# Kernel optimization log

Hardware: AMD Instinct MI355X
Metric: run time of the kernel (lower is better)

Reference implementation:

```python
import math
import jax, jax.numpy as jnp
import numpy as np

THETA = 2.0 ** 16
TWO_PI = 2.0 * math.pi


def _freqs(N):
    # quantize(arange(N), 2) = floor(t/2)*2 -> paired frequencies
    idx = jnp.floor(jnp.arange(N, dtype=jnp.float32) / 2.0) * 2.0
    return 1.0 / (THETA ** (idx / N)) / TWO_PI  # (N,)


def _rope(v, cos, sin):
    # rotate pairs: (-v_odd, v_even) interleaved back to original layout
    v_rot = jnp.stack((-v[..., 1::2], v[..., ::2]), axis=-1).reshape(v.shape)
    return v * cos + v_rot * sin


def setup_inputs() -> dict:
    key = jax.random.key(0)
    k1, k2 = jax.random.split(key)
    B, nh, T, N, D = 1, 4, 2048, 8192, 256
    Q = jax.random.normal(k1, (B, nh, T, N), dtype=jnp.float32) * 0.02
    V = jax.random.normal(k2, (B, 1, T, D), dtype=jnp.float32)
    return {"Q": Q, "V": V}


def reference(Q, V):
    # Q: (B, nh, T, N) sparse neuron space; V: (B, 1, T, D) embedding space; K is Q
    T, N = Q.shape[2], Q.shape[3]
    freqs = _freqs(N)
    phases = jnp.arange(T, dtype=jnp.float32)[:, None] * freqs[None, :]  # (T, N)
    ang = (phases % 1.0) * TWO_PI
    cos, sin = jnp.cos(ang), jnp.sin(ang)
    QR = _rope(Q, cos, sin)  # (B, nh, T, N)
    scores = jnp.einsum('bhtn,bhsn->bhts', QR, QR)  # (B, nh, T, T)
    causal = jnp.tril(jnp.ones((T, T), dtype=bool), k=-1)  # strictly lower
    scores = jnp.where(causal, scores, 0.0)
    # V broadcasts over heads: (B, nh, T, T) @ (B, 1, T, D) -> (B, nh, T, D)
    return jnp.matmul(scores, V)
```

## Files before the change

kernel.cpp:

```cpp
#include <hip/hip_runtime.h>

#define LDS_AS __attribute__((address_space(3)))
#define GLB_AS __attribute__((address_space(1)))

typedef __attribute__((ext_vector_type(8))) short bf16x8;
typedef __attribute__((ext_vector_type(4))) float f32x4;

static constexpr int NH = 4;
static constexpr int T  = 2048;
static constexpr int N  = 8192;
static constexpr int D  = 256;

__device__ inline unsigned short f2bf(float f) {
    unsigned int u = __float_as_uint(f);
    u += 0x7FFFu + ((u >> 16) & 1u);
    return (unsigned short)(u >> 16);
}

__device__ inline void gl2lds16(const void* g, void* l) {
    __builtin_amdgcn_global_load_lds((GLB_AS void*)g, (LDS_AS void*)l, 16, 0, 0);
}

__global__ void rope_kernel(const float* __restrict__ Q, unsigned short* __restrict__ QR) {
    int g = blockIdx.x * 256 + threadIdx.x;
    int base = g << 2;
    int n = base & (N - 1);
    int t = (base >> 13) & (T - 1);
    const float4 q = *(const float4*)(Q + (size_t)base);
    float tf = (float)t;
    const float inv2pi = 0.15915494309189535f;
    float f0 = exp2f((float)n       * (-1.0f / 512.0f)) * inv2pi;
    float f1 = exp2f((float)(n + 2) * (-1.0f / 512.0f)) * inv2pi;
    float r0 = tf * f0; r0 -= floorf(r0);
    float r1 = tf * f1; r1 -= floorf(r1);
    float s0 = __builtin_amdgcn_sinf(r0), c0 = __builtin_amdgcn_cosf(r0);
    float s1 = __builtin_amdgcn_sinf(r1), c1 = __builtin_amdgcn_cosf(r1);
    ushort4 o;
    o.x = f2bf(q.x * c0 - q.y * s0);
    o.y = f2bf(q.y * c0 + q.x * s0);
    o.z = f2bf(q.z * c1 - q.w * s1);
    o.w = f2bf(q.w * c1 + q.z * s1);
    *(ushort4*)(QR + (size_t)base) = o;
}

__global__ void vt_kernel(const float* __restrict__ V, unsigned short* __restrict__ Vt) {
    int g = blockIdx.x * 256 + threadIdx.x;
    int t = g >> 8;
    int d = g & (D - 1);
    Vt[(size_t)d * T + t] = f2bf(V[g]);
}

__global__ __launch_bounds__(256) void gemm1_kernel(const unsigned short* __restrict__ QR,
                                                    unsigned short* __restrict__ S) {
    __shared__ __align__(16) unsigned short As[128 * 32];
    __shared__ __align__(16) unsigned short Bs[128 * 32];

    int bx = blockIdx.x;
    int h = bx / 136, pair = bx % 136;
    int bi = 0;
    while (((bi + 1) * (bi + 2)) / 2 <= pair) bi++;
    int bj = pair - (bi * (bi + 1)) / 2;

    const unsigned short* A = QR + (size_t)h * T * N + (size_t)bi * 128 * N;
    const unsigned short* B = QR + (size_t)h * T * N + (size_t)bj * 128 * N;

    int tid = threadIdx.x;
    int lane = tid & 63, wave = tid >> 6;
    int wm = wave >> 1, wn = wave & 1;
    int quad = lane >> 4, l16 = lane & 15;
    int srow = tid >> 2;
    int scol = (tid & 3) * 8;

    f32x4 acc[4][4];
    #pragma unroll
    for (int i = 0; i < 4; i++)
        #pragma unroll
        for (int j = 0; j < 4; j++)
            #pragma unroll
            for (int r = 0; r < 4; r++) acc[i][j][r] = 0.0f;

    for (int k0 = 0; k0 < N; k0 += 32) {
        __syncthreads();
        gl2lds16(A + (size_t)srow * N + k0 + scol,        &As[srow * 32 + scol]);
        gl2lds16(A + (size_t)(srow + 64) * N + k0 + scol, &As[(srow + 64) * 32 + scol]);
        gl2lds16(B + (size_t)srow * N + k0 + scol,        &Bs[srow * 32 + scol]);
        gl2lds16(B + (size_t)(srow + 64) * N + k0 + scol, &Bs[(srow + 64) * 32 + scol]);
        __syncthreads();

        bf16x8 a[4], b[4];
        #pragma unroll
        for (int i = 0; i < 4; i++) {
            int ra = wm * 64 + i * 16 + l16;
            a[i] = *(const bf16x8*)&As[ra * 32 + quad * 8];
            int rb = wn * 64 + i * 16 + l16;
            b[i] = *(const bf16x8*)&Bs[rb * 32 + quad * 8];
        }
        #pragma unroll
        for (int i = 0; i < 4; i++)
            #pragma unroll
            for (int j = 0; j < 4; j++)
                acc[i][j] = __builtin_amdgcn_mfma_f32_16x16x32_bf16(a[i], b[j], acc[i][j], 0, 0, 0);
    }

    unsigned short* Sh = S + (size_t)h * T * T;
    #pragma unroll
    for (int i = 0; i < 4; i++) {
        int t_base = bi * 128 + wm * 64 + i * 16 + quad * 4;
        #pragma unroll
        for (int j = 0; j < 4; j++) {
            int s_g = bj * 128 + wn * 64 + j * 16 + l16;
            #pragma unroll
            for (int r = 0; r < 4; r++) {
                int t_g = t_base + r;
                float v = (s_g < t_g) ? acc[i][j][r] : 0.0f;
                Sh[(size_t)t_g * T + s_g] = f2bf(v);
            }
        }
    }
}

__global__ __launch_bounds__(256) void gemm2_kernel(const unsigned short* __restrict__ S,
                                                    const unsigned short* __restrict__ Vt,
                                                    float* __restrict__ out) {
    __shared__ __align__(16) unsigned short As[128 * 32];
    __shared__ __align__(16) unsigned short Bs[128 * 32];

    int bx = blockIdx.x;
    int h = bx >> 5;
    int rem = bx & 31;
    int bi = rem >> 1;
    int dblk = rem & 1;

    const unsigned short* A = S + (size_t)h * T * T + (size_t)bi * 128 * T;
    const unsigned short* B = Vt + (size_t)dblk * 128 * T;

    int tid = threadIdx.x;
    int lane = tid & 63, wave = tid >> 6;
    int wm = wave >> 1, wn = wave & 1;
    int quad = lane >> 4, l16 = lane & 15;
    int srow = tid >> 2;
    int scol = (tid & 3) * 8;

    f32x4 acc[4][4];
    #pragma unroll
    for (int i = 0; i < 4; i++)
        #pragma unroll
        for (int j = 0; j < 4; j++)
            #pragma unroll
            for (int r = 0; r < 4; r++) acc[i][j][r] = 0.0f;

    int kend = (bi + 1) * 128;
    for (int k0 = 0; k0 < kend; k0 += 32) {
        __syncthreads();
        gl2lds16(A + (size_t)srow * T + k0 + scol,        &As[srow * 32 + scol]);
        gl2lds16(A + (size_t)(srow + 64) * T + k0 + scol, &As[(srow + 64) * 32 + scol]);
        gl2lds16(B + (size_t)srow * T + k0 + scol,        &Bs[srow * 32 + scol]);
        gl2lds16(B + (size_t)(srow + 64) * T + k0 + scol, &Bs[(srow + 64) * 32 + scol]);
        __syncthreads();

        bf16x8 a[4], b[4];
        #pragma unroll
        for (int i = 0; i < 4; i++) {
            int ra = wm * 64 + i * 16 + l16;
            a[i] = *(const bf16x8*)&As[ra * 32 + quad * 8];
            int rb = wn * 64 + i * 16 + l16;
            b[i] = *(const bf16x8*)&Bs[rb * 32 + quad * 8];
        }
        #pragma unroll
        for (int i = 0; i < 4; i++)
            #pragma unroll
            for (int j = 0; j < 4; j++)
                acc[i][j] = __builtin_amdgcn_mfma_f32_16x16x32_bf16(a[i], b[j], acc[i][j], 0, 0, 0);
    }

    float* oh = out + (size_t)h * T * D;
    #pragma unroll
    for (int i = 0; i < 4; i++) {
        int t_base = bi * 128 + wm * 64 + i * 16 + quad * 4;
        #pragma unroll
        for (int j = 0; j < 4; j++) {
            int d_g = dblk * 128 + wn * 64 + j * 16 + l16;
            #pragma unroll
            for (int r = 0; r < 4; r++) {
                int t_g = t_base + r;
                oh[(size_t)t_g * D + d_g] = acc[i][j][r];
            }
        }
    }
}

extern "C" void kernel_launch(void* const* d_in, const int* in_sizes, int n_in,
                              void* d_out, int out_size, void* d_ws, size_t ws_size,
                              hipStream_t stream) {
    const float* Q = (const float*)d_in[0];
    const float* V = (const float*)d_in[1];
    float* out = (float*)d_out;

    const size_t qr_elems = (size_t)NH * T * N;
    const size_t vt_elems = (size_t)D * T;
    const size_t s_elems  = (size_t)NH * T * T;
    const size_t needed = (qr_elems + vt_elems + s_elems) * sizeof(unsigned short);
    if (ws_size < needed) return;

    unsigned short* QR = (unsigned short*)d_ws;
    unsigned short* Vt = QR + qr_elems;
    unsigned short* S  = Vt + vt_elems;

    rope_kernel<<<(NH * T * N / 4) / 256, 256, 0, stream>>>(Q, QR);
    vt_kernel<<<(T * D) / 256, 256, 0, stream>>>(V, Vt);
    gemm1_kernel<<<NH * 136, 256, 0, stream>>>(QR, S);
    gemm2_kernel<<<NH * 32, 256, 0, stream>>>(S, Vt, out);
}
```

Baseline: 646.9 us.

## Split-K both GEMMs with atomic accumulation and tile the V transpose through LDS

gemm1 now splits the N reduction into KS chunks. Each chunk writes a separate bf16 partial score matrix, which raises the block count from 544 to 1088 on a 256-CU part. gemm2 splits each row block's causal K range into 512-wide chunks and also sums over the KS partials, accumulating into a zeroed output with float atomicAdd to give more parallelism than the original 128 blocks. The V transpose goes through a padded LDS tile so that global accesses coalesce. The cost is double the S workspace traffic, an extra memset, and atomic contention. Each partial is also rounded to bf16 separately, which changes numerics slightly.

```diff
diff --git a/kernel.cpp b/kernel.cpp
--- a/kernel.cpp
+++ b/kernel.cpp
@@ -44,25 +44,45 @@
 }
 
 __global__ void vt_kernel(const float* __restrict__ V, unsigned short* __restrict__ Vt) {
-    int g = blockIdx.x * 256 + threadIdx.x;
-    int t = g >> 8;
-    int d = g & (D - 1);
-    Vt[(size_t)d * T + t] = f2bf(V[g]);
+    __shared__ unsigned short tile[64 * 65];
+    int tb = blockIdx.x >> 2, db = blockIdx.x & 3;
+    int t0 = tb * 64, d0 = db * 64;
+    int tid = threadIdx.x;
+    #pragma unroll
+    for (int r = 0; r < 16; r++) {
+        int idx = tid + r * 256;
+        int tl = idx >> 6, dl = idx & 63;
+        tile[tl * 65 + dl] = f2bf(V[(size_t)(t0 + tl) * D + d0 + dl]);
+    }
+    __syncthreads();
+    #pragma unroll
+    for (int r = 0; r < 16; r++) {
+        int idx = tid + r * 256;
+        int dl = idx >> 6, tl = idx & 63;
+        Vt[(size_t)(d0 + dl) * T + t0 + tl] = tile[tl * 65 + dl];
+    }
 }
 
 __global__ __launch_bounds__(256) void gemm1_kernel(const unsigned short* __restrict__ QR,
-                                                    unsigned short* __restrict__ S) {
+                                                    unsigned short* __restrict__ S, int KS) {
     __shared__ __align__(16) unsigned short As[128 * 32];
     __shared__ __align__(16) unsigned short Bs[128 * 32];
 
     int bx = blockIdx.x;
-    int h = bx / 136, pair = bx % 136;
+    int per_h = 136 * KS;
+    int h = bx / per_h;
+    int rem = bx % per_h;
+    int pair = rem / KS;
+    int ks = rem % KS;
     int bi = 0;
     while (((bi + 1) * (bi + 2)) / 2 <= pair) bi++;
     int bj = pair - (bi * (bi + 1)) / 2;
 
     const unsigned short* A = QR + (size_t)h * T * N + (size_t)bi * 128 * N;
     const unsigned short* B = QR + (size_t)h * T * N + (size_t)bj * 128 * N;
+
+    int KN = N / KS;
+    int k_begin = ks * KN, k_end = k_begin + KN;
 
     int tid = threadIdx.x;
     int lane = tid & 63, wave = tid >> 6;
@@ -79,7 +99,7 @@
             #pragma unroll
             for (int r = 0; r < 4; r++) acc[i][j][r] = 0.0f;
 
-    for (int k0 = 0; k0 < N; k0 += 32) {
+    for (int k0 = k_begin; k0 < k_end; k0 += 32) {
         __syncthreads();
         gl2lds16(A + (size_t)srow * N + k0 + scol,        &As[srow * 32 + scol]);
         gl2lds16(A + (size_t)(srow + 64) * N + k0 + scol, &As[(srow + 64) * 32 + scol]);
@@ -90,10 +110,8 @@
         bf16x8 a[4], b[4];
         #pragma unroll
         for (int i = 0; i < 4; i++) {
-            int ra = wm * 64 + i * 16 + l16;
-            a[i] = *(const bf16x8*)&As[ra * 32 + quad * 8];
-            int rb = wn * 64 + i * 16 + l16;
-            b[i] = *(const bf16x8*)&Bs[rb * 32 + quad * 8];
+            a[i] = *(const bf16x8*)&As[(wm * 64 + i * 16 + l16) * 32 + quad * 8];
+            b[i] = *(const bf16x8*)&Bs[(wn * 64 + i * 16 + l16) * 32 + quad * 8];
         }
         #pragma unroll
         for (int i = 0; i < 4; i++)
@@ -102,7 +120,7 @@
                 acc[i][j] = __builtin_amdgcn_mfma_f32_16x16x32_bf16(a[i], b[j], acc[i][j], 0, 0, 0);
     }
 
-    unsigned short* Sh = S + (size_t)h * T * T;
+    unsigned short* Sh = S + (size_t)ks * NH * T * T + (size_t)h * T * T;
     #pragma unroll
     for (int i = 0; i < 4; i++) {
         int t_base = bi * 128 + wm * 64 + i * 16 + quad * 4;
@@ -121,18 +139,29 @@
 
 __global__ __launch_bounds__(256) void gemm2_kernel(const unsigned short* __restrict__ S,
                                                     const unsigned short* __restrict__ Vt,
-                                                    float* __restrict__ out) {
+                                                    float* __restrict__ out, int KS) {
     __shared__ __align__(16) unsigned short As[128 * 32];
     __shared__ __align__(16) unsigned short Bs[128 * 32];
 
     int bx = blockIdx.x;
-    int h = bx >> 5;
-    int rem = bx & 31;
-    int bi = rem >> 1;
-    int dblk = rem & 1;
-
-    const unsigned short* A = S + (size_t)h * T * T + (size_t)bi * 128 * T;
-    const unsigned short* B = Vt + (size_t)dblk * 128 * T;
+    int per_h = 2 * KS * 40;
+    int h = bx / per_h;
+    int rem = bx % per_h;
+    int dblk = rem / (KS * 40);
+    int rem2 = rem % (KS * 40);
+    int ks = rem2 / 40;
+    int tc = rem2 % 40;
+    int bi = 0, cum = 0;
+    for (; bi < 16; bi++) { int nc = (bi + 4) >> 2; if (cum + nc > tc) break; cum += nc; }
+    int c = tc - cum;
+
+    int kend = (bi + 1) * 128;
+    int cstart = c * 512;
+    int clen = min(512, kend - cstart);
+
+    const unsigned short* A = S + (size_t)ks * NH * T * T + (size_t)h * T * T
+                                + (size_t)bi * 128 * T + cstart;
+    const unsigned short* B = Vt + (size_t)dblk * 128 * T + cstart;
 
     int tid = threadIdx.x;
     int lane = tid & 63, wave = tid >> 6;
@@ -149,8 +178,7 @@
             #pragma unroll
             for (int r = 0; r < 4; r++) acc[i][j][r] = 0.0f;
 
-    int kend = (bi + 1) * 128;
-    for (int k0 = 0; k0 < kend; k0 += 32) {
+    for (int k0 = 0; k0 < clen; k0 += 32) {
         __syncthreads();
         gl2lds16(A + (size_t)srow * T + k0 + scol,        &As[srow * 32 + scol]);
         gl2lds16(A + (size_t)(srow + 64) * T + k0 + scol, &As[(srow + 64) * 32 + scol]);
@@ -161,10 +189,8 @@
         bf16x8 a[4], b[4];
         #pragma unroll
         for (int i = 0; i < 4; i++) {
-            int ra = wm * 64 + i * 16 + l16;
-            a[i] = *(const bf16x8*)&As[ra * 32 + quad * 8];
-            int rb = wn * 64 + i * 16 + l16;
-            b[i] = *(const bf16x8*)&Bs[rb * 32 + quad * 8];
+            a[i] = *(const bf16x8*)&As[(wm * 64 + i * 16 + l16) * 32 + quad * 8];
+            b[i] = *(const bf16x8*)&Bs[(wn * 64 + i * 16 + l16) * 32 + quad * 8];
         }
         #pragma unroll
         for (int i = 0; i < 4; i++)
@@ -183,7 +209,7 @@
             #pragma unroll
             for (int r = 0; r < 4; r++) {
                 int t_g = t_base + r;
-                oh[(size_t)t_g * D + d_g] = acc[i][j][r];
+                atomicAdd(&oh[(size_t)t_g * D + d_g], acc[i][j][r]);
             }
         }
     }
@@ -199,15 +225,17 @@
     const size_t qr_elems = (size_t)NH * T * N;
     const size_t vt_elems = (size_t)D * T;
     const size_t s_elems  = (size_t)NH * T * T;
-    const size_t needed = (qr_elems + vt_elems + s_elems) * sizeof(unsigned short);
-    if (ws_size < needed) return;
+
+    int KS = (ws_size >= (qr_elems + vt_elems + 2 * s_elems) * sizeof(unsigned short)) ? 2 : 1;
+    if (ws_size < (qr_elems + vt_elems + (size_t)KS * s_elems) * sizeof(unsigned short)) return;
 
     unsigned short* QR = (unsigned short*)d_ws;
     unsigned short* Vt = QR + qr_elems;
     unsigned short* S  = Vt + vt_elems;
 
     rope_kernel<<<(NH * T * N / 4) / 256, 256, 0, stream>>>(Q, QR);
-    vt_kernel<<<(T * D) / 256, 256, 0, stream>>>(V, Vt);
-    gemm1_kernel<<<NH * 136, 256, 0, stream>>>(QR, S);
-    gemm2_kernel<<<NH * 32, 256, 0, stream>>>(S, Vt, out);
-}
+    vt_kernel<<<(T / 64) * (D / 64), 256, 0, stream>>>(V, Vt);
+    gemm1_kernel<<<NH * 136 * KS, 256, 0, stream>>>(QR, S, KS);
+    hipMemsetAsync(d_out, 0, (size_t)out_size * sizeof(float), stream);
+    gemm2_kernel<<<NH * 2 * KS * 40, 256, 0, stream>>>(S, Vt, out, KS);
+}
```

New measurement: 622.5 us. 3.8% less time.
